# Kernel tuning notes

Measured on AMD Instinct MI355X. Metric: run time of the kernel, lower is better.

## Reference

```python
import jax, jax.numpy as jnp
import numpy as np

K_HOPS = 3  # spektral TAGConv default
BN_EPS = 1e-3  # keras BatchNormalization default epsilon


def _propagate(x, edge_src, edge_dst, edge_weight, n_nodes):
    # y[dst] += w * x[src]  (sparse adjacency @ x)
    msg = x[edge_src] * edge_weight[:, None]
    return jax.ops.segment_sum(msg, edge_dst, num_segments=n_nodes)


def _tag_conv(x, edge_src, edge_dst, edge_weight, W, b):
    n = x.shape[0]
    hops = [x]
    h = x
    for _ in range(K_HOPS):
        h = _propagate(h, edge_src, edge_dst, edge_weight, n)
        hops.append(h)
    # concat hops along features then dense combine: [N, F*(K+1)] @ [F*(K+1), C]
    return jnp.concatenate(hops, axis=-1) @ W + b


def setup_inputs() -> dict:
    key = jax.random.key(0)
    ks = jax.random.split(key, 6)
    N, F, E, H, L = 20000, 2000, 640000, 128, 15
    x = jax.random.normal(ks[0], (N, F), dtype=jnp.float32)
    edge_src = jax.random.randint(ks[1], (E,), 0, N, dtype=jnp.int32)
    edge_dst = jax.random.randint(ks[2], (E,), 0, N, dtype=jnp.int32)
    # normalized adjacency weights, roughly 1/avg_degree scale
    edge_weight = jax.random.uniform(ks[3], (E,), dtype=jnp.float32) / 32.0
    W1 = jax.random.normal(ks[4], (F * (K_HOPS + 1), H), dtype=jnp.float32) * (1.0 / np.sqrt(F * (K_HOPS + 1)))
    b1 = jnp.zeros((H,), dtype=jnp.float32)
    gamma = jnp.ones((H,), dtype=jnp.float32)
    beta = jnp.zeros((H,), dtype=jnp.float32)
    moving_mean = jnp.zeros((H,), dtype=jnp.float32)
    moving_var = jnp.ones((H,), dtype=jnp.float32)
    W2 = jax.random.normal(ks[5], (H * (K_HOPS + 1), L), dtype=jnp.float32) * (1.0 / np.sqrt(H * (K_HOPS + 1)))
    b2 = jnp.zeros((L,), dtype=jnp.float32)
    return {"x": x, "edge_src": edge_src, "edge_dst": edge_dst, "edge_weight": edge_weight,
            "W1": W1, "b1": b1, "gamma": gamma, "beta": beta,
            "moving_mean": moving_mean, "moving_var": moving_var, "W2": W2, "b2": b2}


def reference(x, edge_src, edge_dst, edge_weight, W1, b1, gamma, beta,
              moving_mean, moving_var, W2, b2):
    # training=False: Dropout is identity, BN uses moving statistics
    h = _tag_conv(x, edge_src, edge_dst, edge_weight, W1, b1)
    h = (h - moving_mean) * jax.lax.rsqrt(moving_var + BN_EPS) * gamma + beta
    h = jax.nn.relu(h)
    z = _tag_conv(h, edge_src, edge_dst, edge_weight, W2, b2)
    return z
```

## Files before the change

### kernel.cpp

```cpp
#include <hip/hip_runtime.h>
#include <hip/hip_bf16.h>
#include <cstdint>
#include <cstddef>

#define N_NODES 20000
#define F_IN    2000
#define H_DIM   128
#define L_DIM   15
#define K_PAD   2048
#define YS      384
#define BM      128
#define BN      64
#define BK      32
#define I_TILES 157

typedef __attribute__((ext_vector_type(4))) float f32x4;
typedef __attribute__((ext_vector_type(8))) short s16x8;
typedef __attribute__((ext_vector_type(8))) unsigned short u16x8;

__device__ __forceinline__ unsigned short f2bf(float f) {
  unsigned int u = __float_as_uint(f);
  u += 0x7fff + ((u >> 16) & 1);
  return (unsigned short)(u >> 16);
}

__device__ __forceinline__ unsigned int pkbf(float a, float b) {
  union { __hip_bfloat162 h; unsigned int u; } cv;
  cv.h = __float22bfloat162_rn(make_float2(a, b));
  return cv.u;
}

__device__ __forceinline__ float2 bf2f(unsigned int u) {
  float2 r;
  r.x = __uint_as_float(u << 16);
  r.y = __uint_as_float(u & 0xffff0000u);
  return r;
}

__global__ __launch_bounds__(256) void k_cvt_x(const float* __restrict__ x,
                                               unsigned short* __restrict__ xb) {
  unsigned int t = blockIdx.x * 256u + threadIdx.x;
  unsigned int row = t >> 8;
  unsigned int colB = (t & 255u) * 8u;
  u16x8 o = {0, 0, 0, 0, 0, 0, 0, 0};
  if (colB < F_IN) {
    const float4 a = *(const float4*)(x + (size_t)row * F_IN + colB);
    const float4 b = *(const float4*)(x + (size_t)row * F_IN + colB + 4);
    o[0] = f2bf(a.x); o[1] = f2bf(a.y); o[2] = f2bf(a.z); o[3] = f2bf(a.w);
    o[4] = f2bf(b.x); o[5] = f2bf(b.y); o[6] = f2bf(b.z); o[7] = f2bf(b.w);
  }
  *(u16x8*)(xb + (size_t)t * 8) = o;
}

__global__ __launch_bounds__(256) void k_cvt_w1(const float* __restrict__ W1,
                                                unsigned short* __restrict__ bt) {
  __shared__ unsigned short tile[128 * 67];
  const int hop = blockIdx.x >> 5;
  const int k0  = (blockIdx.x & 31) * 64;
  const int t = threadIdx.x;
#pragma unroll
  for (int it = 0; it < 8; ++it) {
    int f4 = it * 256 + t;
    int r  = f4 >> 5;
    int c4 = f4 & 31;
    int k = k0 + r;
    float4 v = make_float4(0.f, 0.f, 0.f, 0.f);
    if (k < F_IN) v = *(const float4*)(W1 + (size_t)(hop * F_IN + k) * H_DIM + c4 * 4);
    tile[(c4 * 4 + 0) * 67 + r] = f2bf(v.x);
    tile[(c4 * 4 + 1) * 67 + r] = f2bf(v.y);
    tile[(c4 * 4 + 2) * 67 + r] = f2bf(v.z);
    tile[(c4 * 4 + 3) * 67 + r] = f2bf(v.w);
  }
  __syncthreads();
  const int c = t >> 1, kh = (t & 1) * 32;
  unsigned short* dst = bt + (size_t)(hop * 128 + c) * K_PAD + k0 + kh;
  const unsigned short* srcp = tile + c * 67 + kh;
#pragma unroll
  for (int q = 0; q < 4; ++q) {
    u16x8 o;
#pragma unroll
    for (int e = 0; e < 8; ++e) o[e] = srcp[q * 8 + e];
    *(u16x8*)(dst + q * 8) = o;
  }
}

__global__ __launch_bounds__(256) void k_gemm1(const unsigned short* __restrict__ A,
                                               const unsigned short* __restrict__ B,
                                               float* __restrict__ Y,
                                               unsigned short* __restrict__ Yb3) {
  __shared__ unsigned short As[BM * BK];
  __shared__ unsigned short Bs[BN * BK];
  const int b = blockIdx.x;
  const int i_tile = (b & 7) + 8 * (b >> 6);
  const int j_tile = (b >> 3) & 7;
  if (i_tile >= I_TILES) return;
  const int rowA0 = i_tile * BM;
  const int colB0 = j_tile * BN;
  const int tid  = threadIdx.x;
  const int lane = tid & 63;
  const int wave = tid >> 6;
  const int wm = (wave >> 1) * 64;
  const int wn = (wave & 1) * 32;
  const int quad = lane >> 4;
  const int l15  = lane & 15;
  f32x4 acc[4][2] = {};

  for (int kt = 0; kt < K_PAD; kt += BK) {
#pragma unroll
    for (int r = 0; r < 2; ++r) {
      int c = r * 256 + tid;
      int row = c >> 2;
      int kc = (c & 3) * 8;
      const unsigned short* ga = A + (size_t)(rowA0 + row) * K_PAD + kt + kc;
      __builtin_amdgcn_global_load_lds((const __attribute__((address_space(1))) void*)ga,
                                       (__attribute__((address_space(3))) void*)(As + c * 8),
                                       16, 0, 0);
    }
    {
      int c = tid;
      int row = c >> 2;
      int kc = (c & 3) * 8;
      const unsigned short* gb = B + (size_t)(colB0 + row) * K_PAD + kt + kc;
      __builtin_amdgcn_global_load_lds((const __attribute__((address_space(1))) void*)gb,
                                       (__attribute__((address_space(3))) void*)(Bs + c * 8),
                                       16, 0, 0);
    }
    __syncthreads();
    s16x8 af[4], bfr[2];
#pragma unroll
    for (int i = 0; i < 4; ++i)
      af[i] = *(const s16x8*)(As + (wm + i * 16 + l15) * BK + quad * 8);
#pragma unroll
    for (int j = 0; j < 2; ++j)
      bfr[j] = *(const s16x8*)(Bs + (wn + j * 16 + l15) * BK + quad * 8);
#pragma unroll
    for (int i = 0; i < 4; ++i)
#pragma unroll
      for (int j = 0; j < 2; ++j)
        acc[i][j] = __builtin_amdgcn_mfma_f32_16x16x32_bf16(af[i], bfr[j], acc[i][j], 0, 0, 0);
    __syncthreads();
  }

#pragma unroll
  for (int i = 0; i < 4; ++i) {
    int row0 = rowA0 + wm + i * 16 + quad * 4;
#pragma unroll
    for (int j = 0; j < 2; ++j) {
      int gcol = colB0 + wn + j * 16 + l15;
#pragma unroll
      for (int r = 0; r < 4; ++r) {
        int row = row0 + r;
        if (row < N_NODES) {
          if (j_tile < 6)
            Y[(size_t)row * YS + gcol] = acc[i][j][r];
          else
            Yb3[(size_t)row * H_DIM + (gcol - 384)] = f2bf(acc[i][j][r]);
        }
      }
    }
  }
}

__global__ __launch_bounds__(256) void k_hist(const int* __restrict__ dst,
                                              int* __restrict__ deg, int E) {
  int i = blockIdx.x * 256 + threadIdx.x;
  int e = i * 4;
  if (e + 4 <= E) {
    int4 d4 = *(const int4*)(dst + e);
    atomicAdd(&deg[d4.x], 1); atomicAdd(&deg[d4.y], 1);
    atomicAdd(&deg[d4.z], 1); atomicAdd(&deg[d4.w], 1);
  } else {
    for (; e < E; ++e) atomicAdd(&deg[dst[e]], 1);
  }
}

__global__ __launch_bounds__(1024) void k_scan(const int* __restrict__ deg,
                                               int* __restrict__ rowStart,
                                               int* __restrict__ cursor,
                                               int* __restrict__ realEnd) {
  __shared__ int sums[1024];
  const int t = threadIdx.x;
  const int chunk = (N_NODES + 1023) / 1024;
  int lo = t * chunk;
  int hi = lo + chunk; if (hi > N_NODES) hi = N_NODES;
  int s = 0;
  for (int i = lo; i < hi; ++i) s += (deg[i] + 15) & ~15;
  sums[t] = s;
  __syncthreads();
  for (int off = 1; off < 1024; off <<= 1) {
    int v = sums[t];
    int u = (t >= off) ? sums[t - off] : 0;
    __syncthreads();
    sums[t] = v + u;
    __syncthreads();
  }
  int run = sums[t] - s;
  for (int i = lo; i < hi; ++i) {
    rowStart[i] = run; cursor[i] = run; realEnd[i] = run + deg[i];
    run += (deg[i] + 15) & ~15;
  }
  if (t == 1023) rowStart[N_NODES] = run;
}

__global__ __launch_bounds__(256) void k_scatter(const int* __restrict__ src,
                                                 const int* __restrict__ dst,
                                                 const float* __restrict__ w,
                                                 int* cursor,
                                                 int2* __restrict__ eSW, int E) {
  int e = blockIdx.x * 256 + threadIdx.x;
  if (e >= E) return;
  int p = atomicAdd(&cursor[dst[e]], 1);
  eSW[p] = make_int2(src[e], __float_as_int(w[e]));
}

__global__ __launch_bounds__(256) void k_pad(const int* __restrict__ rowStart,
                                             const int* __restrict__ realEnd,
                                             int2* __restrict__ eSW) {
  int t = blockIdx.x * 256 + threadIdx.x;
  int d = t >> 4, i = t & 15;
  if (d >= N_NODES) return;
  int s = realEnd[d] + i;
  if (s < rowStart[d + 1]) eSW[s] = make_int2(0, 0);
}

__global__ __launch_bounds__(256) void k_prop128f(const int* __restrict__ rowStart,
    const int2* __restrict__ eSW,
    const unsigned short* __restrict__ gsrc,
    const float* __restrict__ addv, int addStride, int addOff,
    unsigned short* __restrict__ outb, float* __restrict__ outf,
    const float* __restrict__ b1, const float* __restrict__ gamma,
    const float* __restrict__ beta, const float* __restrict__ mean,
    const float* __restrict__ var, int doBN) {
  const int lane = threadIdx.x & 63;
  const int wave = threadIdx.x >> 6;
  const int eidx = lane >> 4;
  const int s16  = lane & 15;
  const int d = blockIdx.x * 4 + wave;
  const int s0 = rowStart[d], s1 = rowStart[d + 1];
  f32x4 a0 = {0.f, 0.f, 0.f, 0.f};
  f32x4 a1 = {0.f, 0.f, 0.f, 0.f};

  const int nc = (s1 - s0) >> 4;
  int j = s0;
  int2 ed0[4], ed1[4];
  if (nc > 0) {
#pragma unroll
    for (int i = 0; i < 4; ++i) ed0[i] = eSW[j + 4 * i + eidx];
  }
  for (int c = 0; c < nc; ++c) {
    uint4 g[4];
#pragma unroll
    for (int i = 0; i < 4; ++i)
      g[i] = *(const uint4*)(gsrc + (size_t)ed0[i].x * H_DIM + s16 * 8);
    if (c + 1 < nc) {
#pragma unroll
      for (int i = 0; i < 4; ++i) ed1[i] = eSW[j + 16 + 4 * i + eidx];
    }
#pragma unroll
    for (int i = 0; i < 4; ++i) {
      float w = __int_as_float(ed0[i].y);
      float2 p0 = bf2f(g[i].x), p1 = bf2f(g[i].y);
      float2 p2 = bf2f(g[i].z), p3 = bf2f(g[i].w);
      a0.x = fmaf(w, p0.x, a0.x); a0.y = fmaf(w, p0.y, a0.y);
      a0.z = fmaf(w, p1.x, a0.z); a0.w = fmaf(w, p1.y, a0.w);
      a1.x = fmaf(w, p2.x, a1.x); a1.y = fmaf(w, p2.y, a1.y);
      a1.z = fmaf(w, p3.x, a1.z); a1.w = fmaf(w, p3.y, a1.w);
    }
#pragma unroll
    for (int i = 0; i < 4; ++i) ed0[i] = ed1[i];
    j += 16;
  }
  a0.x += __shfl_xor(a0.x, 16); a0.y += __shfl_xor(a0.y, 16);
  a0.z += __shfl_xor(a0.z, 16); a0.w += __shfl_xor(a0.w, 16);
  a1.x += __shfl_xor(a1.x, 16); a1.y += __shfl_xor(a1.y, 16);
  a1.z += __shfl_xor(a1.z, 16); a1.w += __shfl_xor(a1.w, 16);
  a0.x += __shfl_xor(a0.x, 32); a0.y += __shfl_xor(a0.y, 32);
  a0.z += __shfl_xor(a0.z, 32); a0.w += __shfl_xor(a0.w, 32);
  a1.x += __shfl_xor(a1.x, 32); a1.y += __shfl_xor(a1.y, 32);
  a1.z += __shfl_xor(a1.z, 32); a1.w += __shfl_xor(a1.w, 32);
  if (lane >= 16) return;
  const int c8 = s16 * 8;
  const float* ap = addv + (size_t)d * addStride + addOff + c8;
  float4 av0 = *(const float4*)ap;
  float4 av1 = *(const float4*)(ap + 4);
  float r0 = av0.x + a0.x, r1 = av0.y + a0.y, r2 = av0.z + a0.z, r3 = av0.w + a0.w;
  float r4 = av1.x + a1.x, r5 = av1.y + a1.y, r6 = av1.z + a1.z, r7 = av1.w + a1.w;
  if (doBN) {
    float4 bb0 = *(const float4*)(b1 + c8),    bb1 = *(const float4*)(b1 + c8 + 4);
    float4 gg0 = *(const float4*)(gamma + c8), gg1 = *(const float4*)(gamma + c8 + 4);
    float4 be0 = *(const float4*)(beta + c8),  be1 = *(const float4*)(beta + c8 + 4);
    float4 mm0 = *(const float4*)(mean + c8),  mm1 = *(const float4*)(mean + c8 + 4);
    float4 vv0 = *(const float4*)(var + c8),   vv1 = *(const float4*)(var + c8 + 4);
    r0 = (r0 + bb0.x - mm0.x) * rsqrtf(vv0.x + 1e-3f) * gg0.x + be0.x;
    r1 = (r1 + bb0.y - mm0.y) * rsqrtf(vv0.y + 1e-3f) * gg0.y + be0.y;
    r2 = (r2 + bb0.z - mm0.z) * rsqrtf(vv0.z + 1e-3f) * gg0.z + be0.z;
    r3 = (r3 + bb0.w - mm0.w) * rsqrtf(vv0.w + 1e-3f) * gg0.w + be0.w;
    r4 = (r4 + bb1.x - mm1.x) * rsqrtf(vv1.x + 1e-3f) * gg1.x + be1.x;
    r5 = (r5 + bb1.y - mm1.y) * rsqrtf(vv1.y + 1e-3f) * gg1.y + be1.y;
    r6 = (r6 + bb1.z - mm1.z) * rsqrtf(vv1.z + 1e-3f) * gg1.z + be1.z;
    r7 = (r7 + bb1.w - mm1.w) * rsqrtf(vv1.w + 1e-3f) * gg1.w + be1.w;
    r0 = r0 > 0.f ? r0 : 0.f; r1 = r1 > 0.f ? r1 : 0.f;
    r2 = r2 > 0.f ? r2 : 0.f; r3 = r3 > 0.f ? r3 : 0.f;
    r4 = r4 > 0.f ? r4 : 0.f; r5 = r5 > 0.f ? r5 : 0.f;
    r6 = r6 > 0.f ? r6 : 0.f; r7 = r7 > 0.f ? r7 : 0.f;
    float* op = outf + (size_t)d * H_DIM + c8;
    *(float4*)op = make_float4(r0, r1, r2, r3);
    *(float4*)(op + 4) = make_float4(r4, r5, r6, r7);
  } else {
    *(uint4*)(outb + (size_t)d * H_DIM + c8) =
        make_uint4(pkbf(r0, r1), pkbf(r2, r3), pkbf(r4, r5), pkbf(r6, r7));
  }
}

__global__ __launch_bounds__(256) void k_gemm2(const float* __restrict__ Hh,
                                               const float* __restrict__ W2,
                                               float* __restrict__ Y2) {
  __shared__ float w2s[512 * 15];
  for (int i = threadIdx.x; i < 512 * 15; i += 256) w2s[i] = W2[i];
  __syncthreads();
  const int c = threadIdx.x & 63;
  const int d = blockIdx.x * 4 + (threadIdx.x >> 6);
  if (c >= 60 || d >= N_NODES) return;
  const int hop = c / 15, j = c % 15;
  const float4* hr4 = (const float4*)(Hh + (size_t)d * H_DIM);
  float acc = 0.f;
#pragma unroll 8
  for (int k4 = 0; k4 < 32; ++k4) {
    float4 h = hr4[k4];
    const float* wp = w2s + ((hop << 7) + k4 * 4) * 15 + j;
    acc = fmaf(h.x, wp[0],  acc);
    acc = fmaf(h.y, wp[15], acc);
    acc = fmaf(h.z, wp[30], acc);
    acc = fmaf(h.w, wp[45], acc);
  }
  Y2[(size_t)d * 60 + c] = acc;
}

__global__ __launch_bounds__(256) void k_prop15(const int* __restrict__ rowStart,
    const int2* __restrict__ eSW,
    const float* __restrict__ in, int inStride, int inOff,
    const float* __restrict__ addv, int addStride, int addOff,
    const float* __restrict__ bias, float* __restrict__ out) {
  const int f = threadIdx.x & 15;
  const int d = blockIdx.x * 16 + (threadIdx.x >> 4);
  if (f >= 15) return;
  const int s0 = rowStart[d], s1 = rowStart[d + 1];
  float acc = 0.f;
  int j = s0;
  for (; j + 4 <= s1; j += 4) {
    int2 e0 = eSW[j], e1 = eSW[j + 1], e2 = eSW[j + 2], e3 = eSW[j + 3];
    float v0 = in[(size_t)e0.x * inStride + inOff + f];
    float v1 = in[(size_t)e1.x * inStride + inOff + f];
    float v2 = in[(size_t)e2.x * inStride + inOff + f];
    float v3 = in[(size_t)e3.x * inStride + inOff + f];
    acc = fmaf(__int_as_float(e0.y), v0, acc);
    acc = fmaf(__int_as_float(e1.y), v1, acc);
    acc = fmaf(__int_as_float(e2.y), v2, acc);
    acc = fmaf(__int_as_float(e3.y), v3, acc);
  }
  for (; j < s1; ++j) {
    int2 e = eSW[j];
    acc = fmaf(__int_as_float(e.y), in[(size_t)e.x * inStride + inOff + f], acc);
  }
  float b = bias ? bias[f] : 0.f;
  out[(size_t)d * 15 + f] = addv[(size_t)d * addStride + addOff + f] + acc + b;
}

extern "C" void kernel_launch(void* const* d_in, const int* in_sizes, int n_in,
                              void* d_out, int out_size, void* d_ws, size_t ws_size,
                              hipStream_t stream) {
  const float* x     = (const float*)d_in[0];
  const int*   esrc  = (const int*)d_in[1];
  const int*   edst  = (const int*)d_in[2];
  const float* ew    = (const float*)d_in[3];
  const float* W1    = (const float*)d_in[4];
  const float* b1    = (const float*)d_in[5];
  const float* gamma = (const float*)d_in[6];
  const float* beta  = (const float*)d_in[7];
  const float* mmean = (const float*)d_in[8];
  const float* mvar  = (const float*)d_in[9];
  const float* W2    = (const float*)d_in[10];
  const float* b2    = (const float*)d_in[11];
  const int E = in_sizes[1];
  char* ws = (char*)d_ws;

  unsigned short* xb  = (unsigned short*)(ws);
  float*          Y   = (float*)(ws + 81920000);
  unsigned short* Yb3 = (unsigned short*)(ws + 112640000);
  unsigned short* w1r = (unsigned short*)(ws + 117760000);
  int2*           eSW = (int2*)(ws + 119857152);
  int*       deg      = (int*)(ws + 127537152);
  int*       rowStart = (int*)(ws + 127617280);
  int*       cursor   = (int*)(ws + 127697408);
  int*       realEnd  = (int*)(ws + 127777536);
  unsigned short* P   = (unsigned short*)(ws);
  unsigned short* Q   = (unsigned short*)(ws + 5120000);
  float*          Hb  = (float*)(ws + 10240000);
  float*          Y2  = (float*)(ws + 20480000);
  float*          zP  = (float*)(ws + 25280000);
  float*          zQ  = (float*)(ws + 26480000);
  float*          zout = (float*)d_out;

  hipMemsetAsync(deg, 0, N_NODES * sizeof(int), stream);

  k_hist<<<(E / 4 + 255) / 256 + 1, 256, 0, stream>>>(edst, deg, E);
  k_scan<<<1, 1024, 0, stream>>>(deg, rowStart, cursor, realEnd);
  k_scatter<<<(E + 255) / 256, 256, 0, stream>>>(esrc, edst, ew, cursor, eSW, E);
  k_pad<<<(N_NODES * 16) / 256, 256, 0, stream>>>(rowStart, realEnd, eSW);

  k_cvt_x<<<(N_NODES * K_PAD / 8) / 256, 256, 0, stream>>>(x, xb);
  k_cvt_w1<<<128, 256, 0, stream>>>(W1, w1r);
  k_gemm1<<<1280, 256, 0, stream>>>(xb, w1r, Y, Yb3);

  k_prop128f<<<N_NODES / 4, 256, 0, stream>>>(rowStart, eSW, Yb3, Y, YS, 256,
                                              P, nullptr, b1, gamma, beta, mmean, mvar, 0);
  k_prop128f<<<N_NODES / 4, 256, 0, stream>>>(rowStart, eSW, P, Y, YS, 128,
                                              Q, nullptr, b1, gamma, beta, mmean, mvar, 0);
  k_prop128f<<<N_NODES / 4, 256, 0, stream>>>(rowStart, eSW, Q, Y, YS, 0,
                                              nullptr, Hb, b1, gamma, beta, mmean, mvar, 1);

  k_gemm2<<<N_NODES / 4, 256, 0, stream>>>(Hb, W2, Y2);
  k_prop15<<<N_NODES / 16, 256, 0, stream>>>(rowStart, eSW, Y2, 60, 45, Y2, 60, 30, nullptr, zP);
  k_prop15<<<N_NODES / 16, 256, 0, stream>>>(rowStart, eSW, zP, 15, 0, Y2, 60, 15, nullptr, zQ);
  k_prop15<<<N_NODES / 16, 256, 0, stream>>>(rowStart, eSW, zQ, 15, 0, Y2, 60, 0, b2, zout);
}
```

Before: 582.6 us.

## Swizzle GEMM1 operand layout against LDS bank conflicts; pad layer-2 features to 16

The bf16 x and W1 conversion kernels now write each 32-element k chunk with an XOR swizzle keyed on the row. The GEMM reads its LDS fragments through the same swizzle, so the ds_read_b128 fragment loads avoid bank conflicts without padding LDS. Separately, layer-2 intermediates are padded from 15 to 16 floats per row. The 15-wide propagation kernel is rewritten as one wave per node: 16 edges are processed in parallel with float4 gathers, edge records are prefetched, and a shuffle reduction combines the partial sums. This changes the padding-free edge loop's assumption: it only handles full multiples of 16 edges, so it relies on the padded CSR layout.

```diff
diff --git a/kernel.cpp b/kernel.cpp
--- a/kernel.cpp
+++ b/kernel.cpp
@@ -13,6 +13,8 @@
 #define BN      64
 #define BK      32
 #define I_TILES 157
+
+#define FSW(r) (((r) + ((r) >> 2)) & 3)
 
 typedef __attribute__((ext_vector_type(4))) float f32x4;
 typedef __attribute__((ext_vector_type(8))) short s16x8;
@@ -49,7 +51,9 @@
     o[0] = f2bf(a.x); o[1] = f2bf(a.y); o[2] = f2bf(a.z); o[3] = f2bf(a.w);
     o[4] = f2bf(b.x); o[5] = f2bf(b.y); o[6] = f2bf(b.z); o[7] = f2bf(b.w);
   }
-  *(u16x8*)(xb + (size_t)t * 8) = o;
+  unsigned int s  = (colB >> 3) & 3;
+  unsigned int sp = s ^ FSW(row & 15);
+  *(u16x8*)(xb + (size_t)row * K_PAD + (colB & ~31u) + sp * 8) = o;
 }
 
 __global__ __launch_bounds__(256) void k_cvt_w1(const float* __restrict__ W1,
@@ -73,6 +77,7 @@
   }
   __syncthreads();
   const int c = t >> 1, kh = (t & 1) * 32;
+  const int fN = FSW(c & 15);
   unsigned short* dst = bt + (size_t)(hop * 128 + c) * K_PAD + k0 + kh;
   const unsigned short* srcp = tile + c * 67 + kh;
 #pragma unroll
@@ -80,7 +85,7 @@
     u16x8 o;
 #pragma unroll
     for (int e = 0; e < 8; ++e) o[e] = srcp[q * 8 + e];
-    *(u16x8*)(dst + q * 8) = o;
+    *(u16x8*)(dst + (q ^ fN) * 8) = o;
   }
 }
 
@@ -103,6 +108,7 @@
   const int wn = (wave & 1) * 32;
   const int quad = lane >> 4;
   const int l15  = lane & 15;
+  const int qs   = (quad ^ FSW(l15)) * 8;
   f32x4 acc[4][2] = {};
 
   for (int kt = 0; kt < K_PAD; kt += BK) {
@@ -129,10 +135,10 @@
     s16x8 af[4], bfr[2];
 #pragma unroll
     for (int i = 0; i < 4; ++i)
-      af[i] = *(const s16x8*)(As + (wm + i * 16 + l15) * BK + quad * 8);
+      af[i] = *(const s16x8*)(As + (wm + i * 16 + l15) * BK + qs);
 #pragma unroll
     for (int j = 0; j < 2; ++j)
-      bfr[j] = *(const s16x8*)(Bs + (wn + j * 16 + l15) * BK + quad * 8);
+      bfr[j] = *(const s16x8*)(Bs + (wn + j * 16 + l15) * BK + qs);
 #pragma unroll
     for (int i = 0; i < 4; ++i)
 #pragma unroll
@@ -333,37 +339,54 @@
     acc = fmaf(h.z, wp[30], acc);
     acc = fmaf(h.w, wp[45], acc);
   }
-  Y2[(size_t)d * 60 + c] = acc;
-}
-
-__global__ __launch_bounds__(256) void k_prop15(const int* __restrict__ rowStart,
+  Y2[(size_t)d * 64 + hop * 16 + j] = acc;
+}
+
+__global__ __launch_bounds__(256) void k_prop15g(const int* __restrict__ rowStart,
     const int2* __restrict__ eSW,
     const float* __restrict__ in, int inStride, int inOff,
     const float* __restrict__ addv, int addStride, int addOff,
-    const float* __restrict__ bias, float* __restrict__ out) {
-  const int f = threadIdx.x & 15;
-  const int d = blockIdx.x * 16 + (threadIdx.x >> 4);
-  if (f >= 15) return;
+    const float* __restrict__ bias, float* __restrict__ out, int outStride) {
+  const int lane = threadIdx.x & 63;
+  const int wave = threadIdx.x >> 6;
+  const int eidx = lane >> 2, fc = lane & 3;
+  const int d = blockIdx.x * 4 + wave;
   const int s0 = rowStart[d], s1 = rowStart[d + 1];
-  float acc = 0.f;
+  float4 acc = make_float4(0.f, 0.f, 0.f, 0.f);
+  const int nc = (s1 - s0) >> 4;
   int j = s0;
-  for (; j + 4 <= s1; j += 4) {
-    int2 e0 = eSW[j], e1 = eSW[j + 1], e2 = eSW[j + 2], e3 = eSW[j + 3];
-    float v0 = in[(size_t)e0.x * inStride + inOff + f];
-    float v1 = in[(size_t)e1.x * inStride + inOff + f];
-    float v2 = in[(size_t)e2.x * inStride + inOff + f];
-    float v3 = in[(size_t)e3.x * inStride + inOff + f];
-    acc = fmaf(__int_as_float(e0.y), v0, acc);
-    acc = fmaf(__int_as_float(e1.y), v1, acc);
-    acc = fmaf(__int_as_float(e2.y), v2, acc);
-    acc = fmaf(__int_as_float(e3.y), v3, acc);
-  }
-  for (; j < s1; ++j) {
-    int2 e = eSW[j];
-    acc = fmaf(__int_as_float(e.y), in[(size_t)e.x * inStride + inOff + f], acc);
-  }
-  float b = bias ? bias[f] : 0.f;
-  out[(size_t)d * 15 + f] = addv[(size_t)d * addStride + addOff + f] + acc + b;
+  int2 ed = make_int2(0, 0);
+  if (nc > 0) ed = eSW[j + eidx];
+  for (int c = 0; c < nc; ++c) {
+    float4 g = *(const float4*)(in + (size_t)ed.x * inStride + inOff + fc * 4);
+    int2 edn = ed;
+    if (c + 1 < nc) edn = eSW[j + 16 + eidx];
+    float w = __int_as_float(ed.y);
+    acc.x = fmaf(w, g.x, acc.x); acc.y = fmaf(w, g.y, acc.y);
+    acc.z = fmaf(w, g.z, acc.z); acc.w = fmaf(w, g.w, acc.w);
+    ed = edn; j += 16;
+  }
+#pragma unroll
+  for (int m = 4; m <= 32; m <<= 1) {
+    acc.x += __shfl_xor(acc.x, m); acc.y += __shfl_xor(acc.y, m);
+    acc.z += __shfl_xor(acc.z, m); acc.w += __shfl_xor(acc.w, m);
+  }
+  if (lane >= 4) return;
+  float4 av = *(const float4*)(addv + (size_t)d * addStride + addOff + fc * 4);
+  float r0 = av.x + acc.x, r1 = av.y + acc.y, r2 = av.z + acc.z, r3 = av.w + acc.w;
+  if (outStride == 16) {
+    *(float4*)(out + (size_t)d * 16 + fc * 4) = make_float4(r0, r1, r2, r3);
+  } else {
+    float* op = out + (size_t)d * 15 + fc * 4;
+    if (fc < 3) {
+      float4 bb = *(const float4*)(bias + fc * 4);
+      *(float4*)op = make_float4(r0 + bb.x, r1 + bb.y, r2 + bb.z, r3 + bb.w);
+    } else {
+      op[0] = r0 + bias[12];
+      op[1] = r1 + bias[13];
+      op[2] = r2 + bias[14];
+    }
+  }
 }
 
 extern "C" void kernel_launch(void* const* d_in, const int* in_sizes, int n_in,
@@ -397,8 +420,8 @@
   unsigned short* Q   = (unsigned short*)(ws + 5120000);
   float*          Hb  = (float*)(ws + 10240000);
   float*          Y2  = (float*)(ws + 20480000);
-  float*          zP  = (float*)(ws + 25280000);
-  float*          zQ  = (float*)(ws + 26480000);
+  float*          zP  = (float*)(ws + 25600000);
+  float*          zQ  = (float*)(ws + 26880000);
   float*          zout = (float*)d_out;
 
   hipMemsetAsync(deg, 0, N_NODES * sizeof(int), stream);
@@ -420,7 +443,7 @@
                                               nullptr, Hb, b1, gamma, beta, mmean, mvar, 1);
 
   k_gemm2<<<N_NODES / 4, 256, 0, stream>>>(Hb, W2, Y2);
-  k_prop15<<<N_NODES / 16, 256, 0, stream>>>(rowStart, eSW, Y2, 60, 45, Y2, 60, 30, nullptr, zP);
-  k_prop15<<<N_NODES / 16, 256, 0, stream>>>(rowStart, eSW, zP, 15, 0, Y2, 60, 15, nullptr, zQ);
-  k_prop15<<<N_NODES / 16, 256, 0, stream>>>(rowStart, eSW, zQ, 15, 0, Y2, 60, 0, b2, zout);
-}
+  k_prop15g<<<N_NODES / 4, 256, 0, stream>>>(rowStart, eSW, Y2, 64, 48, Y2, 64, 32, nullptr, zP, 16);
+  k_prop15g<<<N_NODES / 4, 256, 0, stream>>>(rowStart, eSW, zP, 16, 0, Y2, 64, 16, nullptr, zQ, 16);
+  k_prop15g<<<N_NODES / 4, 256, 0, stream>>>(rowStart, eSW, zQ, 16, 0, Y2, 64, 0, b2, zout, 15);
+}
```

Result: no change. 583.8 us (+0.2%).
